# Kernel optimization log

Hardware: AMD Instinct MI355X
Metric: run time of the kernel (lower is better)

Reference implementation:

```python
import jax, jax.numpy as jnp
import numpy as np

V, E, H, M, B, S = 32000, 512, 1024, 256, 2, 1024
GC = 24  # smear_gate_channels = min(24, embedding_dim)


def setup_inputs() -> dict:
    key = jax.random.key(0)
    ks = jax.random.split(key, 20)
    s = 0.02
    return {
        "input_ids": jax.random.randint(ks[0], (B, S), 0, V),
        "emb": jax.random.normal(ks[1], (V, E)) * s,
        "W_ih": jax.random.normal(ks[2], (3 * H, E)) * s,
        "W_hh": jax.random.normal(ks[3], (3 * H, H)) * s,
        "b_ih": jax.random.normal(ks[4], (3 * H,)) * s,
        "b_hh": jax.random.normal(ks[5], (3 * H,)) * s,
        "Wq": jax.random.normal(ks[6], (M, H)) * s,
        "bq": jax.random.normal(ks[7], (M,)) * s,
        "Wk": jax.random.normal(ks[8], (M, H)) * s,
        "bk": jax.random.normal(ks[9], (M,)) * s,
        "Wg": jax.random.normal(ks[10], (1, H)) * s,
        "bg": jax.random.normal(ks[11], (1,)) * s,
        "Whe": jax.random.normal(ks[12], (E, H)) * s,
        "bhe": jax.random.normal(ks[13], (E,)) * s,
        "out_bias": jax.random.normal(ks[14], (V,)) * s,
        "memory_scale": jnp.float32(6.0),
        "smear_W": jax.random.normal(ks[15], (1, GC)) * s,
        "smear_lambda": jax.random.normal(ks[16], (1,)) * 0.1,
    }


def forward(input_ids, emb, W_ih, W_hh, b_ih, b_hh, Wq, bq, Wk, bk, Wg, bg,
            Whe, bhe, out_bias, memory_scale, smear_W, smear_lambda):
    x = emb[input_ids]  # (B,S,E)
    # smear: gated copy of previous token embedding into current
    sg = smear_lambda * jax.nn.sigmoid(x[:, 1:, :GC] @ smear_W.T)  # (B,S-1,1)
    x = jnp.concatenate([x[:, :1], x[:, 1:] + sg * x[:, :-1]], axis=1)
    # GRU (PyTorch gate order r,z,n); precompute input projections
    xg = x @ W_ih.T + b_ih  # (B,S,3H)

    def step(h, xg_t):
        xr, xz, xn = jnp.split(xg_t, 3, axis=-1)
        hg = h @ W_hh.T + b_hh
        hr, hz, hn = jnp.split(hg, 3, axis=-1)
        r = jax.nn.sigmoid(xr + hr)
        z = jax.nn.sigmoid(xz + hz)
        n = jnp.tanh(xn + r * hn)
        h_new = (1.0 - z) * n + z * h
        return h_new, h_new

    h0 = jnp.zeros((x.shape[0], H), dtype=x.dtype)
    _, states = jax.lax.scan(step, h0, jnp.swapaxes(xg, 0, 1))
    states = jnp.swapaxes(states, 0, 1)  # (B,S,H); dropout is identity at eval
    # tied output projection
    base_logits = (states @ Whe.T + bhe) @ emb.T + out_bias  # (B,S,V)
    q = states @ Wq.T + bq  # (B,S,M)
    k = states @ Wk.T + bk
    scores = jnp.einsum("bsm,btm->bst", q, k) / jnp.sqrt(jnp.float32(M))
    mask = jnp.tril(jnp.ones((S, S), dtype=bool), k=-1)[None]  # (1,S,S)
    scores = jnp.where(mask, scores, jnp.finfo(scores.dtype).min)
    attn = jax.nn.softmax(scores, axis=-1) * mask
    attn = attn / jnp.maximum(attn.sum(axis=-1, keepdims=True), 1e-6)
    g = jax.nn.sigmoid(states @ Wg.T + bg)  # (B,S,1)
    gated = attn * (g * memory_scale)  # (B,S,S)
    # scatter_add gated attention into vocab logits at input_ids positions
    b_idx = jnp.arange(B)[:, None, None]
    s_idx = jnp.arange(S)[None, :, None]
    v_idx = input_ids[:, None, :]  # broadcasts to (B,S,S)
    base_logits = base_logits.at[b_idx, s_idx, v_idx].add(gated)
    return base_logits


def reference(input_ids, emb, W_ih, W_hh, b_ih, b_hh, Wq, bq, Wk, bk, Wg, bg,
              Whe, bhe, out_bias, memory_scale, smear_W, smear_lambda):
    return forward(input_ids, emb, W_ih, W_hh, b_ih, b_hh, Wq, bq, Wk, bk,
                   Wg, bg, Whe, bhe, out_bias, memory_scale, smear_W, smear_lambda)
```

## Files before the change

### kernel.cpp

```cpp
#include <hip/hip_runtime.h>
#include <stdint.h>

#define V_ 32000
#define E_ 512
#define H_ 1024
#define M_ 256
#define B_ 2
#define S_ 1024
#define GC_ 24

typedef unsigned short u16;
typedef unsigned int u32;
typedef unsigned long long u64;

typedef __attribute__((ext_vector_type(8))) short short8;
typedef __attribute__((ext_vector_type(4))) float floatx4;
typedef __attribute__((ext_vector_type(2))) float floatx2;
typedef __attribute__((ext_vector_type(2))) _Float16 halfx2;

__device__ __forceinline__ float bf2f(u16 u){ return __uint_as_float(((u32)u) << 16); }
__device__ __forceinline__ float bflo(u32 u){ return __uint_as_float(u << 16); }
__device__ __forceinline__ float bfhi(u32 u){ return __uint_as_float(u & 0xffff0000u); }
__device__ __forceinline__ u16 f2bf(float f){
  u32 u = __float_as_uint(f);
  u32 r = (u + 0x7fffu + ((u >> 16) & 1u)) >> 16;
  return (u16)r;
}
__device__ __forceinline__ float sigm(float x){ return 1.f / (1.f + __expf(-x)); }

__device__ __forceinline__ float dot2f16(u32 a, u32 b, float c){
#if __has_builtin(__builtin_amdgcn_fdot2)
  return __builtin_amdgcn_fdot2(__builtin_bit_cast(halfx2, a),
                                __builtin_bit_cast(halfx2, b), c, false);
#else
  halfx2 av = __builtin_bit_cast(halfx2, a);
  halfx2 bv = __builtin_bit_cast(halfx2, b);
  return fmaf((float)av.y, (float)bv.y, fmaf((float)av.x, (float)bv.x, c));
#endif
}

__device__ __forceinline__ void gload_lds16(const void* g, void* l){
  __builtin_amdgcn_global_load_lds(
      (const __attribute__((address_space(1))) void*)g,
      (__attribute__((address_space(3))) void*)l, 16, 0, 0);
}

__global__ __launch_bounds__(64) void detect_kernel(const u32* __restrict__ emb,
    int* __restrict__ flag, float* __restrict__ scal,
    const void* __restrict__ lam, const void* __restrict__ ms)
{
  int lane = threadIdx.x;
  int c = 0;
  for (int i = lane; i < 256; i += 64){
    u32 w = emb[i];
    float a = fabsf(__uint_as_float((w & 0xffffu) << 16));
    if (a > 1e-5f && a < 1.0f) c++;
  }
  #pragma unroll
  for (int o = 32; o; o >>= 1) c += __shfl_down(c, o, 64);
  if (lane == 0){
    int isf32 = (c < 128) ? 1 : 0;
    *flag = isf32;
    if (isf32) scal[0] = ((const float*)lam)[0];
    else {
      float v = bf2f(((const u16*)lam)[0]);
      scal[0] = (fabsf(v) <= 4.0f) ? v : ((const float*)lam)[0];
    }
    if (isf32) scal[1] = ((const float*)ms)[0];
    else {
      u16 a = ((const u16*)ms)[0];
      float v = bf2f(a);
      scal[1] = (a != 0 && fabsf(v) > 1e-4f && fabsf(v) < 1e4f) ? v : ((const float*)ms)[0];
    }
  }
}

struct ConvArgs { const void* s[15]; };

#define CONV_TOTAL 22191385
__global__ __launch_bounds__(256) void convall_kernel(ConvArgs a, char* __restrict__ ws,
                                                      const int* __restrict__ flag)
{
  static const int    ns[15]    = {16384000, 1572864, 3145728, 262144, 262144, 1024,
                                   524288, 3072, 3072, 256, 256, 1, 512, 32000, 24};
  static const size_t doffs[15] = {33280, 32801280, 35947008, 42238464, 42762752,
                                   43287040, 43289088, 44337664, 44343808, 44349952,
                                   44350464, 44350976, 44351232, 44352256, 44416512};
  int gid = blockIdx.x * 256 + threadIdx.x;
  if (gid >= CONV_TOTAL) return;
  int isf32 = *flag;
  int seg = -1, r = gid;
  #pragma unroll
  for (int k = 0; k < 15; k++){
    if (seg < 0){ if (r < ns[k]) seg = k; else r -= ns[k]; }
  }
  const void* src = a.s[seg];
  u16* dst = (u16*)(ws + doffs[seg]);
  if (seg == 2){
    float v = isf32 ? ((const float*)src)[r] : bf2f(((const u16*)src)[r]);
    dst[r] = __builtin_bit_cast(u16, (_Float16)v);
  } else {
    dst[r] = isf32 ? f2bf(((const float*)src)[r]) : ((const u16*)src)[r];
  }
}

__global__ __launch_bounds__(64) void smear_kernel(const int* __restrict__ ids,
    const u16* __restrict__ emb, const u16* __restrict__ smW,
    const float* __restrict__ scal, u16* __restrict__ xs)
{
  int row = blockIdx.x;
  int t = row & (S_ - 1);
  int lane = threadIdx.x;
  int id = ids[row];
  const u16* er = emb + (size_t)id * E_;
  float sg = 0.f;
  if (t > 0){
    float p = 0.f;
    if (lane < GC_) p = bf2f(er[lane]) * bf2f(smW[lane]);
    #pragma unroll
    for (int o = 32; o; o >>= 1) p += __shfl_down(p, o, 64);
    float dot = __shfl(p, 0, 64);
    sg = scal[0] * sigm(dot);
  }
  uint4 cur = ((const uint4*)er)[lane];
  uint4 outv = cur;
  if (t > 0){
    const u16* ep = emb + (size_t)ids[row - 1] * E_;
    uint4 prv = ((const uint4*)ep)[lane];
    const u16* cu = (const u16*)&cur;
    const u16* pu = (const u16*)&prv;
    u16* po = (u16*)&outv;
    #pragma unroll
    for (int j = 0; j < 8; j++) po[j] = f2bf(bf2f(cu[j]) + sg * bf2f(pu[j]));
  }
  ((uint4*)(xs + (size_t)row * E_))[lane] = outv;
}

template<bool OUT_BF16>
__global__ __launch_bounds__(256) void gemm_bt(
    const u16* __restrict__ A, const u16* __restrict__ Bm,
    const u16* __restrict__ bias, void* __restrict__ Cout,
    int K, int Ndim)
{
  int wave = threadIdx.x >> 6, lane = threadIdx.x & 63;
  int wm = wave >> 1, wn = wave & 1;
  int m0 = blockIdx.y * 128 + wm * 64;
  int n0 = blockIdx.x * 128 + wn * 64;
  int lrow = lane & 15, lq = lane >> 4;
  floatx4 acc[4][4];
  #pragma unroll
  for (int i = 0; i < 4; i++)
    #pragma unroll
    for (int j = 0; j < 4; j++) acc[i][j] = (floatx4)0.f;
  const u16* Ab = A + (size_t)(m0 + lrow) * K + lq * 8;
  const u16* Bb = Bm + (size_t)(n0 + lrow) * K + lq * 8;
  for (int k0 = 0; k0 < K; k0 += 32){
    short8 af[4], bfr[4];
    #pragma unroll
    for (int tt = 0; tt < 4; tt++)
      af[tt] = *(const short8*)(Ab + (size_t)tt * 16 * K + k0);
    #pragma unroll
    for (int tt = 0; tt < 4; tt++)
      bfr[tt] = *(const short8*)(Bb + (size_t)tt * 16 * K + k0);
    #pragma unroll
    for (int im = 0; im < 4; im++)
      #pragma unroll
      for (int in = 0; in < 4; in++)
        acc[im][in] = __builtin_amdgcn_mfma_f32_16x16x32_bf16(af[im], bfr[in], acc[im][in], 0, 0, 0);
  }
  #pragma unroll
  for (int in = 0; in < 4; in++){
    int n = n0 + in * 16 + lrow;
    float bv = bf2f(bias[n]);
    #pragma unroll
    for (int im = 0; im < 4; im++){
      int mb = m0 + im * 16 + lq * 4;
      #pragma unroll
      for (int r = 0; r < 4; r++){
        float v = acc[im][in][r] + bv;
        size_t off = (size_t)(mb + r) * Ndim + n;
        if (OUT_BF16) ((u16*)Cout)[off] = f2bf(v);
        else          ((float*)Cout)[off] = v;
      }
    }
  }
}

__global__ __launch_bounds__(256) void gemm_v(
    const u16* __restrict__ A, const u16* __restrict__ Bm,
    const u16* __restrict__ bias, float* __restrict__ Cout,
    int K, int Ndim)
{
  __shared__ u16 la[128 * 32];
  __shared__ u16 lb[128 * 32];
  int wave = threadIdx.x >> 6, lane = threadIdx.x & 63;
  int wm = wave >> 1, wn = wave & 1;
  int tm0 = blockIdx.y * 128, tn0 = blockIdx.x * 128;
  int m0 = tm0 + wm * 64;
  int n0 = tn0 + wn * 64;
  int lrow = lane & 15, lq = lane >> 4;
  floatx4 acc[4][4];
  #pragma unroll
  for (int i = 0; i < 4; i++)
    #pragma unroll
    for (int j = 0; j < 4; j++) acc[i][j] = (floatx4)0.f;

  const int o = wave * 1024 + lane * 16;
  for (int k0 = 0; k0 < K; k0 += 32){
    #pragma unroll
    for (int j = 0; j < 2; j++){
      int oo = o + j * 4096;
      int row = oo >> 6;
      int ce  = (oo & 63) >> 1;
      gload_lds16(&A[(size_t)(tm0 + row) * K + k0 + ce],  &la[(wave * 1024 + j * 4096) >> 1]);
      gload_lds16(&Bm[(size_t)(tn0 + row) * K + k0 + ce], &lb[(wave * 1024 + j * 4096) >> 1]);
    }
    __syncthreads();
    short8 af[4], bfr[4];
    #pragma unroll
    for (int tt = 0; tt < 4; tt++)
      af[tt] = *(const short8*)&la[(wm * 64 + tt * 16 + lrow) * 32 + lq * 8];
    #pragma unroll
    for (int tt = 0; tt < 4; tt++)
      bfr[tt] = *(const short8*)&lb[(wn * 64 + tt * 16 + lrow) * 32 + lq * 8];
    #pragma unroll
    for (int im = 0; im < 4; im++)
      #pragma unroll
      for (int in = 0; in < 4; in++)
        acc[im][in] = __builtin_amdgcn_mfma_f32_16x16x32_bf16(af[im], bfr[in], acc[im][in], 0, 0, 0);
    __syncthreads();
  }
  #pragma unroll
  for (int in = 0; in < 4; in++){
    int n = n0 + in * 16 + lrow;
    float bv = bf2f(bias[n]);
    #pragma unroll
    for (int im = 0; im < 4; im++){
      int mb = m0 + im * 16 + lq * 4;
      #pragma unroll
      for (int r = 0; r < 4; r++)
        Cout[(size_t)(mb + r) * Ndim + n] = acc[im][in][r] + bv;
    }
  }
}

__global__ __launch_bounds__(1024) void gru_kernel(
    const float* __restrict__ xg, const u16* __restrict__ W_hh,
    const u16* __restrict__ b_hh, u32* __restrict__ hslot,
    u16* __restrict__ states)
{
  const int b = blockIdx.x >> 5;
  const int ibase = (blockIdx.x & 31) * 32;
  const int tid = threadIdx.x;
  const int kg = tid >> 5;
  const int il = tid & 31;
  const int i = ibase + il;
  const int w = tid >> 6;

  __shared__ u32   lds_hpk[2][H_ / 2];
  __shared__ float red[3][16][32];

  uint4 Wv[3][4];
  #pragma unroll
  for (int g = 0; g < 3; g++){
    const uint4* p = (const uint4*)(W_hh + ((size_t)(g * H_ + i)) * H_ + kg * 32);
    #pragma unroll
    for (int q = 0; q < 4; q++) Wv[g][q] = p[q];
  }

  float ho = 0.f, xr0 = 0.f, xz0 = 0.f, xn0 = 0.f, bh0 = 0.f, bh1 = 0.f, bh2 = 0.f;
  if (tid < 32){
    bh0 = bf2f(b_hh[ibase + tid]);
    bh1 = bf2f(b_hh[H_ + ibase + tid]);
    bh2 = bf2f(b_hh[2 * H_ + ibase + tid]);
    size_t base = ((size_t)(b * S_)) * 3072 + ibase + tid;
    xr0 = xg[base]; xz0 = xg[base + 1024]; xn0 = xg[base + 2048];
  }

  for (int t = 0; t < S_; t++){
    const int p = t & 1;
    if (tid < 512){
      const u64* rp = (const u64*)(hslot + ((size_t)((p ^ 1) * B_ + b)) * H_) + tid;
      const u32 tg = (u32)t;
      u64 u0;
      do {
        u0 = __hip_atomic_load(rp, __ATOMIC_RELAXED, __HIP_MEMORY_SCOPE_AGENT);
      } while ((((u32)(u0 >> 16) & 0xffffu) != tg) | (((u32)(u0 >> 48)) != tg));
      lds_hpk[p][tid] = ((u32)u0 & 0xffffu) | (((u32)(u0 >> 32)) << 16);
    }
    __syncthreads();
    const u32* hp = &lds_hpk[p][kg * 16];
    float pr = 0.f, pz = 0.f, pn = 0.f;
    #pragma unroll
    for (int q = 0; q < 4; q++){
      uint4 wr = Wv[0][q], wz = Wv[1][q], wn4 = Wv[2][q];
      u32 cr[4] = {wr.x, wr.y, wr.z, wr.w};
      u32 cz[4] = {wz.x, wz.y, wz.z, wz.w};
      u32 cn[4] = {wn4.x, wn4.y, wn4.z, wn4.w};
      #pragma unroll
      for (int e = 0; e < 4; e++){
        u32 h2 = hp[q * 4 + e];
        pr = dot2f16(cr[e], h2, pr);
        pz = dot2f16(cz[e], h2, pz);
        pn = dot2f16(cn[e], h2, pn);
      }
    }
    pr += __shfl_xor(pr, 32, 64);
    pz += __shfl_xor(pz, 32, 64);
    pn += __shfl_xor(pn, 32, 64);
    if ((tid & 63) < 32){
      red[0][w][il] = pr; red[1][w][il] = pz; red[2][w][il] = pn;
    }
    __syncthreads();
    if (tid < 32){
      __builtin_amdgcn_s_setprio(1);
      float hr = 0.f, hz = 0.f, hn = 0.f;
      #pragma unroll
      for (int ww = 0; ww < 16; ww++){
        hr += red[0][ww][tid]; hz += red[1][ww][tid]; hn += red[2][ww][tid];
      }
      float r = sigm(xr0 + hr + bh0);
      float z = sigm(xz0 + hz + bh1);
      float xx = xn0 + r * (hn + bh2);
      float ax = fabsf(xx);
      float et = __expf(-2.f * ax);
      float n = copysignf((1.f - et) * __builtin_amdgcn_rcpf(1.f + et), xx);
      float hnew = (1.f - z) * n + z * ho;
      ho = hnew;
      u16 h16 = __builtin_bit_cast(u16, (_Float16)hnew);
      u32 tgv = (((u32)(t + 1)) << 16) | (u32)h16;
      __hip_atomic_store(&hslot[((size_t)(p * B_ + b)) * H_ + ibase + tid], tgv,
                         __ATOMIC_RELAXED, __HIP_MEMORY_SCOPE_AGENT);
      __builtin_amdgcn_s_setprio(0);
      states[((size_t)(b * S_ + t)) * H_ + ibase + tid] = f2bf(hnew);
      if (t + 1 < S_){
        size_t base = ((size_t)(b * S_ + t + 1)) * 3072 + ibase + tid;
        xr0 = xg[base]; xz0 = xg[base + 1024]; xn0 = xg[base + 2048];
      }
    }
  }
}

__global__ __launch_bounds__(256) void gk_kernel(const u16* __restrict__ states,
    const u16* __restrict__ Wg, const u16* __restrict__ bg, float* __restrict__ gws)
{
  int row = blockIdx.x * 4 + (threadIdx.x >> 6);
  int lane = threadIdx.x & 63;
  const u16* sr = states + (size_t)row * H_;
  float p = 0.f;
  #pragma unroll
  for (int j = 0; j < 16; j++){
    int c = j * 64 + lane;
    p += bf2f(sr[c]) * bf2f(Wg[c]);
  }
  #pragma unroll
  for (int o = 32; o; o >>= 1) p += __shfl_xor(p, o, 64);
  if (lane == 0) gws[row] = sigm(p + bf2f(bg[0]));
}

__global__ __launch_bounds__(1024) void sort_kernel(const int* __restrict__ ids, int* __restrict__ sorted)
{
  int b = blockIdx.x, tid = threadIdx.x;
  __shared__ int arr[S_];
  arr[tid] = (ids[b * S_ + tid] << 11) | tid;
  __syncthreads();
  for (int k = 2; k <= S_; k <<= 1){
    for (int j = k >> 1; j > 0; j >>= 1){
      int ixj = tid ^ j;
      if (ixj > tid){
        int a = arr[tid], c = arr[ixj];
        bool dir = (tid & k) == 0;
        if (dir ? (a > c) : (a < c)){ arr[tid] = c; arr[ixj] = a; }
      }
      __syncthreads();
    }
  }
  sorted[b * S_ + tid] = arr[tid];
}

__global__ __launch_bounds__(256) void attn_kernel(
    const float* __restrict__ scores, const float* __restrict__ gws,
    const float* __restrict__ scal, float* __restrict__ gated)
{
  int s = blockIdx.x, b = blockIdx.y;
  if (s == 0) return;
  int tid = threadIdx.x;
  __shared__ float rbm[4], rbs[4];
  const float* srow = scores + ((size_t)(b * S_ + s)) * S_;
  float myS[4];
  float lmax = -1e30f;
  #pragma unroll
  for (int r = 0; r < 4; r++){
    int t = tid + 256 * r;
    if (t < s){
      float d = srow[t] * 0.0625f;
      myS[r] = d;
      lmax = fmaxf(lmax, d);
    }
  }
  #pragma unroll
  for (int o = 32; o; o >>= 1) lmax = fmaxf(lmax, __shfl_xor(lmax, o, 64));
  if ((tid & 63) == 0) rbm[tid >> 6] = lmax;
  __syncthreads();
  float gmax = fmaxf(fmaxf(rbm[0], rbm[1]), fmaxf(rbm[2], rbm[3]));
  float lsum = 0.f;
  #pragma unroll
  for (int r = 0; r < 4; r++){
    int t = tid + 256 * r;
    if (t < s){ myS[r] = __expf(myS[r] - gmax); lsum += myS[r]; }
  }
  #pragma unroll
  for (int o = 32; o; o >>= 1) lsum += __shfl_xor(lsum, o, 64);
  if ((tid & 63) == 0) rbs[tid >> 6] = lsum;
  __syncthreads();
  float gsum = rbs[0] + rbs[1] + rbs[2] + rbs[3];
  float fac = gws[b * S_ + s] * scal[1] / gsum;
  float* grow = gated + ((size_t)(b * S_ + s)) * S_;
  #pragma unroll
  for (int r = 0; r < 4; r++){
    int t = tid + 256 * r;
    if (t < s) grow[t] = myS[r] * fac;
  }
}

__global__ __launch_bounds__(256) void scatter_kernel(
    const int* __restrict__ sorted, const float* __restrict__ gated,
    float* __restrict__ out)
{
  int gid = blockIdx.x * 256 + threadIdx.x;
  int e = gid & (S_ - 1);
  int row = gid >> 10;
  int s = row & (S_ - 1);
  int b = row >> 10;
  const int* sb = sorted + b * S_;
  int pk = sb[e];
  int v = pk >> 11;
  if (e > 0 && (sb[e - 1] >> 11) == v) return;
  const float* grow = gated + (size_t)row * S_;
  float sum = 0.f; bool any = false;
  for (int j = e; j < S_; j++){
    int pj = sb[j];
    if ((pj >> 11) != v) break;
    int t = pj & 2047;
    if (t < s){ sum += grow[t]; any = true; }
  }
  if (any){
    size_t off = (size_t)row * V_ + v;
    out[off] += sum;
  }
}

extern "C" void kernel_launch(void* const* d_in, const int* in_sizes, int n_in,
                              void* d_out, int out_size, void* d_ws, size_t ws_size,
                              hipStream_t stream)
{
  const int*  ids   = (const int*)d_in[0];
  const void* emb   = d_in[1];
  const void* W_ih  = d_in[2];
  const void* W_hh  = d_in[3];
  const void* b_ih  = d_in[4];
  const void* b_hh  = d_in[5];
  const void* Wq    = d_in[6];
  const void* bq    = d_in[7];
  const void* Wk    = d_in[8];
  const void* bk    = d_in[9];
  const void* Wg    = d_in[10];
  const void* bg    = d_in[11];
  const void* Whe   = d_in[12];
  const void* bhe   = d_in[13];
  const void* obias = d_in[14];
  const void* ms    = d_in[15];
  const void* smW   = d_in[16];
  const void* lam   = d_in[17];
  (void)in_sizes; (void)n_in; (void)out_size; (void)ws_size;

  char* ws = (char*)d_ws;
  int*   flag   = (int*)(ws + 0);
  float* scal   = (float*)(ws + 256);
  u32*   hslot  = (u32*)(ws + 512);
  u16*   zbias  = (u16*)(ws + 16896);
  u16*   c_emb  = (u16*)(ws + 33280);
  u16*   c_Wih  = (u16*)(ws + 32801280);
  u16*   c_Whh  = (u16*)(ws + 35947008);
  u16*   c_Wq   = (u16*)(ws + 42238464);
  u16*   c_Wk   = (u16*)(ws + 42762752);
  u16*   c_Wg   = (u16*)(ws + 43287040);
  u16*   c_Whe  = (u16*)(ws + 43289088);
  u16*   c_bih  = (u16*)(ws + 44337664);
  u16*   c_bhh  = (u16*)(ws + 44343808);
  u16*   c_bq   = (u16*)(ws + 44349952);
  u16*   c_bk   = (u16*)(ws + 44350464);
  u16*   c_bg   = (u16*)(ws + 44350976);
  u16*   c_bhe  = (u16*)(ws + 44351232);
  u16*   c_ob   = (u16*)(ws + 44352256);
  u16*   c_smW  = (u16*)(ws + 44416512);
  u16*   xs     = (u16*)(ws + 44416768);
  float* xg     = (float*)(ws + 46513920);
  u16*   states = (u16*)(ws + 71679744);
  u16*   hs     = (u16*)(ws + 75874048);
  u16*   qb     = (u16*)(ws + 77971200);
  u16*   kb     = (u16*)(ws + 79019776);
  float* gws    = (float*)(ws + 80068352);
  float* gated  = (float*)(ws + 80076544);
  int*   sorted = (int*)(ws + 88465152);
  float* scores = xg;
  float* out = (float*)d_out;

  hipMemsetAsync(hslot, 0, 16384, stream);
  hipMemsetAsync(zbias, 0, 2048, stream);
  detect_kernel<<<dim3(1), dim3(64), 0, stream>>>((const u32*)emb, flag, scal, lam, ms);

  ConvArgs ca;
  ca.s[0] = emb;  ca.s[1] = W_ih; ca.s[2] = W_hh; ca.s[3] = Wq;   ca.s[4] = Wk;
  ca.s[5] = Wg;   ca.s[6] = Whe;  ca.s[7] = b_ih; ca.s[8] = b_hh; ca.s[9] = bq;
  ca.s[10] = bk;  ca.s[11] = bg;  ca.s[12] = bhe; ca.s[13] = obias; ca.s[14] = smW;
  convall_kernel<<<dim3((CONV_TOTAL + 255) / 256), dim3(256), 0, stream>>>(ca, ws, flag);

  smear_kernel<<<dim3(B_ * S_), dim3(64), 0, stream>>>(ids, c_emb, c_smW, scal, xs);
  gemm_bt<false><<<dim3(3072 / 128, 2048 / 128), dim3(256), 0, stream>>>(xs, c_Wih, c_bih, (void*)xg, E_, 3072);
  gru_kernel<<<dim3(64), dim3(1024), 0, stream>>>(xg, c_Whh, c_bhh, hslot, states);
  gemm_bt<true><<<dim3(512 / 128, 16), dim3(256), 0, stream>>>(states, c_Whe, c_bhe, (void*)hs, H_, 512);
  gemm_bt<true><<<dim3(256 / 128, 16), dim3(256), 0, stream>>>(states, c_Wq, c_bq, (void*)qb, H_, 256);
  gemm_bt<true><<<dim3(256 / 128, 16), dim3(256), 0, stream>>>(states, c_Wk, c_bk, (void*)kb, H_, 256);
  gemm_bt<false><<<dim3(S_ / 128, S_ / 128), dim3(256), 0, stream>>>(qb, kb, zbias, (void*)scores, M_, S_);
  gemm_bt<false><<<dim3(S_ / 128, S_ / 128), dim3(256), 0, stream>>>(qb + (size_t)S_ * M_, kb + (size_t)S_ * M_,
                                                                     zbias, (void*)(scores + (size_t)S_ * S_), M_, S_);
  gk_kernel<<<dim3(512), dim3(256), 0, stream>>>(states, c_Wg, c_bg, gws);
  sort_kernel<<<dim3(B_), dim3(1024), 0, stream>>>(ids, sorted);
  attn_kernel<<<dim3(S_, B_), dim3(256), 0, stream>>>(scores, gws, scal, gated);
  gemm_v<<<dim3(V_ / 128, 16), dim3(256), 0, stream>>>(hs, c_emb, c_ob, out, E_, V_);
  scatter_kernel<<<dim3(B_ * S_ * S_ / 256), dim3(256), 0, stream>>>(sorted, gated, out);
}
```

Before: 2.528 ms.

## Fuse attention softmax with scatter and fold sort into GRU launch

Merges the softmax/gating kernel with the vocab scatter so gated attention rows stay in shared memory instead of round-tripping through an 8 MB global buffer, with sorted ids also cached in LDS. The bitonic sort now runs as two extra blocks of the GRU launch, so it overlaps with the sequential recurrence instead of being a separate launch. The vocab GEMM grid is transposed so consecutive blocks walk along M for a fixed vocab tile, which changes L2 reuse of the embedding tiles. The risk is that extra blocks in the GRU launch could interfere with its residency or progress assumptions.

```diff
diff --git a/kernel.cpp b/kernel.cpp
--- a/kernel.cpp
+++ b/kernel.cpp
@@ -195,7 +195,7 @@
   __shared__ u16 lb[128 * 32];
   int wave = threadIdx.x >> 6, lane = threadIdx.x & 63;
   int wm = wave >> 1, wn = wave & 1;
-  int tm0 = blockIdx.y * 128, tn0 = blockIdx.x * 128;
+  int tm0 = blockIdx.x * 128, tn0 = blockIdx.y * 128;
   int m0 = tm0 + wm * 64;
   int n0 = tn0 + wn * 64;
   int lrow = lane & 15, lq = lane >> 4;
@@ -247,8 +247,28 @@
 __global__ __launch_bounds__(1024) void gru_kernel(
     const float* __restrict__ xg, const u16* __restrict__ W_hh,
     const u16* __restrict__ b_hh, u32* __restrict__ hslot,
-    u16* __restrict__ states)
-{
+    u16* __restrict__ states, const int* __restrict__ ids, int* __restrict__ sorted)
+{
+  __shared__ int arr[S_];
+  if (blockIdx.x >= 64){
+    int b = blockIdx.x - 64, tid = threadIdx.x;
+    arr[tid] = (ids[b * S_ + tid] << 11) | tid;
+    __syncthreads();
+    for (int k = 2; k <= S_; k <<= 1){
+      for (int j = k >> 1; j > 0; j >>= 1){
+        int ixj = tid ^ j;
+        if (ixj > tid){
+          int a = arr[tid], c = arr[ixj];
+          bool dir = (tid & k) == 0;
+          if (dir ? (a > c) : (a < c)){ arr[tid] = c; arr[ixj] = a; }
+        }
+        __syncthreads();
+      }
+    }
+    sorted[b * S_ + tid] = arr[tid];
+    return;
+  }
+
   const int b = blockIdx.x >> 5;
   const int ibase = (blockIdx.x & 31) * 32;
   const int tid = threadIdx.x;
@@ -358,35 +378,20 @@
   if (lane == 0) gws[row] = sigm(p + bf2f(bg[0]));
 }
 
-__global__ __launch_bounds__(1024) void sort_kernel(const int* __restrict__ ids, int* __restrict__ sorted)
-{
-  int b = blockIdx.x, tid = threadIdx.x;
-  __shared__ int arr[S_];
-  arr[tid] = (ids[b * S_ + tid] << 11) | tid;
-  __syncthreads();
-  for (int k = 2; k <= S_; k <<= 1){
-    for (int j = k >> 1; j > 0; j >>= 1){
-      int ixj = tid ^ j;
-      if (ixj > tid){
-        int a = arr[tid], c = arr[ixj];
-        bool dir = (tid & k) == 0;
-        if (dir ? (a > c) : (a < c)){ arr[tid] = c; arr[ixj] = a; }
-      }
-      __syncthreads();
-    }
-  }
-  sorted[b * S_ + tid] = arr[tid];
-}
-
-__global__ __launch_bounds__(256) void attn_kernel(
+__global__ __launch_bounds__(256) void attn_scatter_kernel(
     const float* __restrict__ scores, const float* __restrict__ gws,
-    const float* __restrict__ scal, float* __restrict__ gated)
+    const float* __restrict__ scal, const int* __restrict__ sorted,
+    float* __restrict__ out)
 {
   int s = blockIdx.x, b = blockIdx.y;
   if (s == 0) return;
   int tid = threadIdx.x;
+  __shared__ float grow[S_];
+  __shared__ int   sb[S_];
   __shared__ float rbm[4], rbs[4];
   const float* srow = scores + ((size_t)(b * S_ + s)) * S_;
+  #pragma unroll
+  for (int r = 0; r < 4; r++) sb[tid + 256 * r] = sorted[b * S_ + tid + 256 * r];
   float myS[4];
   float lmax = -1e30f;
   #pragma unroll
@@ -415,38 +420,27 @@
   __syncthreads();
   float gsum = rbs[0] + rbs[1] + rbs[2] + rbs[3];
   float fac = gws[b * S_ + s] * scal[1] / gsum;
-  float* grow = gated + ((size_t)(b * S_ + s)) * S_;
   #pragma unroll
   for (int r = 0; r < 4; r++){
     int t = tid + 256 * r;
     if (t < s) grow[t] = myS[r] * fac;
   }
-}
-
-__global__ __launch_bounds__(256) void scatter_kernel(
-    const int* __restrict__ sorted, const float* __restrict__ gated,
-    float* __restrict__ out)
-{
-  int gid = blockIdx.x * 256 + threadIdx.x;
-  int e = gid & (S_ - 1);
-  int row = gid >> 10;
-  int s = row & (S_ - 1);
-  int b = row >> 10;
-  const int* sb = sorted + b * S_;
-  int pk = sb[e];
-  int v = pk >> 11;
-  if (e > 0 && (sb[e - 1] >> 11) == v) return;
-  const float* grow = gated + (size_t)row * S_;
-  float sum = 0.f; bool any = false;
-  for (int j = e; j < S_; j++){
-    int pj = sb[j];
-    if ((pj >> 11) != v) break;
-    int t = pj & 2047;
-    if (t < s){ sum += grow[t]; any = true; }
-  }
-  if (any){
-    size_t off = (size_t)row * V_ + v;
-    out[off] += sum;
+  __syncthreads();
+  float* orow = out + ((size_t)(b * S_ + s)) * V_;
+  #pragma unroll
+  for (int r = 0; r < 4; r++){
+    int e = tid + 256 * r;
+    int pk = sb[e];
+    int v = pk >> 11;
+    if (e > 0 && (sb[e - 1] >> 11) == v) continue;
+    float sum = 0.f; bool any = false;
+    for (int j = e; j < S_; j++){
+      int pj = sb[j];
+      if ((pj >> 11) != v) break;
+      int t = pj & 2047;
+      if (t < s){ sum += grow[t]; any = true; }
+    }
+    if (any) orow[v] += sum;
   }
 }
 
@@ -501,7 +495,6 @@
   u16*   qb     = (u16*)(ws + 77971200);
   u16*   kb     = (u16*)(ws + 79019776);
   float* gws    = (float*)(ws + 80068352);
-  float* gated  = (float*)(ws + 80076544);
   int*   sorted = (int*)(ws + 88465152);
   float* scores = xg;
   float* out = (float*)d_out;
@@ -518,7 +511,7 @@
 
   smear_kernel<<<dim3(B_ * S_), dim3(64), 0, stream>>>(ids, c_emb, c_smW, scal, xs);
   gemm_bt<false><<<dim3(3072 / 128, 2048 / 128), dim3(256), 0, stream>>>(xs, c_Wih, c_bih, (void*)xg, E_, 3072);
-  gru_kernel<<<dim3(64), dim3(1024), 0, stream>>>(xg, c_Whh, c_bhh, hslot, states);
+  gru_kernel<<<dim3(66), dim3(1024), 0, stream>>>(xg, c_Whh, c_bhh, hslot, states, ids, sorted);
   gemm_bt<true><<<dim3(512 / 128, 16), dim3(256), 0, stream>>>(states, c_Whe, c_bhe, (void*)hs, H_, 512);
   gemm_bt<true><<<dim3(256 / 128, 16), dim3(256), 0, stream>>>(states, c_Wq, c_bq, (void*)qb, H_, 256);
   gemm_bt<true><<<dim3(256 / 128, 16), dim3(256), 0, stream>>>(states, c_Wk, c_bk, (void*)kb, H_, 256);
@@ -526,8 +519,6 @@
   gemm_bt<false><<<dim3(S_ / 128, S_ / 128), dim3(256), 0, stream>>>(qb + (size_t)S_ * M_, kb + (size_t)S_ * M_,
                                                                      zbias, (void*)(scores + (size_t)S_ * S_), M_, S_);
   gk_kernel<<<dim3(512), dim3(256), 0, stream>>>(states, c_Wg, c_bg, gws);
-  sort_kernel<<<dim3(B_), dim3(1024), 0, stream>>>(ids, sorted);
-  attn_kernel<<<dim3(S_, B_), dim3(256), 0, stream>>>(scores, gws, scal, gated);
-  gemm_v<<<dim3(V_ / 128, 16), dim3(256), 0, stream>>>(hs, c_emb, c_ob, out, E_, V_);
-  scatter_kernel<<<dim3(B_ * S_ * S_ / 256), dim3(256), 0, stream>>>(sorted, gated, out);
-}
+  gemm_v<<<dim3(16, V_ / 128), dim3(256), 0, stream>>>(hs, c_emb, c_ob, out, E_, V_);
+  attn_scatter_kernel<<<dim3(S_, B_), dim3(256), 0, stream>>>(scores, gws, scal, sorted, out);
+}
```

After: 2.484 ms. No clear change (-1.7%).
